# Kernel tuning notes

Hardware: AMD Instinct MI355X
Metric: run time of the kernel (lower is better)

## Reference

```python
import jax, jax.numpy as jnp
import numpy as np

EMB = 1024
FF = 4096
NE = 8
TOPK = 2
TEMP = 1.0


def setup_inputs() -> dict:
    key = jax.random.key(0)
    ks = jax.random.split(key, 8)
    s_emb = 1.0 / np.sqrt(EMB)
    s_ff = 1.0 / np.sqrt(FF)
    x = jax.random.normal(ks[0], (4, 2048, EMB), dtype=jnp.float32)
    gate_W = jax.random.uniform(ks[1], (EMB, NE), minval=-s_emb, maxval=s_emb, dtype=jnp.float32)
    gate_b = jax.random.uniform(ks[2], (NE,), minval=-s_emb, maxval=s_emb, dtype=jnp.float32)
    W1 = jax.random.uniform(ks[3], (NE, EMB, FF), minval=-s_emb, maxval=s_emb, dtype=jnp.float32)
    b1 = jax.random.uniform(ks[4], (NE, FF), minval=-s_emb, maxval=s_emb, dtype=jnp.float32)
    W2 = jax.random.uniform(ks[5], (NE, FF, EMB), minval=-s_ff, maxval=s_ff, dtype=jnp.float32)
    b2 = jax.random.uniform(ks[6], (NE, EMB), minval=-s_ff, maxval=s_ff, dtype=jnp.float32)
    return {"x": x, "gate_W": gate_W, "gate_b": gate_b, "W1": W1, "b1": b1, "W2": W2, "b2": b2}


def reference(x, gate_W, gate_b, W1, b1, W2, b2):
    B, S, D = x.shape
    xf = x.reshape(-1, D)  # [T, D]
    T = xf.shape[0]

    gate_logits = (xf @ gate_W + gate_b) / TEMP            # [T, E]
    gate_scores = jax.nn.softmax(gate_logits, axis=-1)     # [T, E]
    topk_scores, topk_idx = jax.lax.top_k(gate_scores, TOPK)
    topk_scores = topk_scores / jnp.sum(topk_scores, axis=-1, keepdims=True)

    # combine_weights[t, e] = sum_i topk_scores[t, i] * (topk_idx[t, i] == e)
    onehot = jax.nn.one_hot(topk_idx, NE, dtype=xf.dtype)  # [T, K, E]
    combine = jnp.einsum('tk,tke->te', topk_scores, onehot)  # [T, E]

    # Dense per-expert FFN (dropout is identity in eval): h = gelu(x W1 + b1); y = h W2 + b2
    h = jax.nn.gelu(jnp.einsum('td,edf->etf', xf, W1) + b1[:, None, :], approximate=False)
    y = jnp.einsum('etf,efd->etd', h, W2) + b2[:, None, :]  # [E, T, D]
    out = jnp.einsum('te,etd->td', combine, y).reshape(B, S, D)

    # Load-balance auxiliary loss
    expert_counts = jnp.sum(onehot, axis=(0, 1))            # [E]
    expert_fraction = expert_counts / (T * TOPK)
    routing_weights = jnp.mean(gate_scores, axis=0)
    aux_loss = NE * jnp.sum(expert_fraction * routing_weights)
    return out, aux_loss
```

## Files before the change

kernel.cpp:

```cpp
#include <hip/hip_runtime.h>
#include <math.h>

#define EMB 1024
#define FF  4096
#define NE  8
#define TTOK 8192

typedef __attribute__((ext_vector_type(4))) float  f32x4;
typedef __attribute__((ext_vector_type(8))) __bf16 bf16x8;

#define MAXROWS  18432

#define WS_COUNTS  0
#define WS_CURSORS 1024
#define WS_SSUM    1056
#define WS_NTILES  2080
#define WS_BASE    2084
#define WS_TILE_E  2176
#define WS_TILE_RB 2816
#define WS_TKIDX   4096
#define WS_TKW     69632
#define WS_SLOT    135168
#define WS_TOKID   200704
#define WS_ROWW    274432
#define WS_BIG2    350208

#define SZ_W1T ((size_t)NE * EMB * FF * 2)
#define SZ_W2T ((size_t)NE * EMB * FF * 2)
#define SZ_XB  ((size_t)TTOK * EMB * 2)
#define SZ_H   ((size_t)MAXROWS * FF * 2)
#define SZ_Y   ((size_t)MAXROWS * EMB * 4)

__device__ inline f32x4 fzero() { f32x4 v = {0.f, 0.f, 0.f, 0.f}; return v; }

__device__ __forceinline__ void gl16(const void* g, void* l) {
    __builtin_amdgcn_global_load_lds(
        (const __attribute__((address_space(1))) void*)g,
        (__attribute__((address_space(3))) void*)l, 16, 0, 0);
}

#define DSR(dst, addr, off) \
    asm volatile("ds_read_b128 %0, %1 offset:" #off : "=v"(dst) : "v"(addr))

__device__ __forceinline__ float gelu_f(float v) {
    float u = fabsf(v) * 0.70710678118654752f;
    float p = 1.0f + u * (0.278393f + u * (0.230389f + u * (0.000972f + u * 0.078108f)));
    p = p * p; p = p * p;
    float er = 1.0f - 1.0f / p;
    float s = (v >= 0.0f) ? er : -er;
    return 0.5f * v * (1.0f + s);
}

__global__ __launch_bounds__(256) void gate_kernel(
    const float* __restrict__ x, const float* __restrict__ gW, const float* __restrict__ gb,
    int* counts, float* ssum, int* tk_idx, float* tk_w)
{
    int wave = threadIdx.x >> 6;
    int lane = threadIdx.x & 63;
    int t = blockIdx.x * 4 + wave;

    float acc[NE];
#pragma unroll
    for (int e = 0; e < NE; e++) acc[e] = 0.f;

    const float* xr = x + (size_t)t * EMB;
#pragma unroll
    for (int i = 0; i < 4; i++) {
        int d0 = i * 256 + lane * 4;
        f32x4 xv = *(const f32x4*)(xr + d0);
#pragma unroll
        for (int j = 0; j < 4; j++) {
            const float* wrow = gW + (size_t)(d0 + j) * NE;
            float xs = xv[j];
#pragma unroll
            for (int e = 0; e < NE; e++) acc[e] += xs * wrow[e];
        }
    }
#pragma unroll
    for (int e = 0; e < NE; e++) {
#pragma unroll
        for (int off = 32; off; off >>= 1) acc[e] += __shfl_xor(acc[e], off, 64);
    }
    if (lane == 0) {
        float sc[NE];
        float m = -1e30f;
        for (int e = 0; e < NE; e++) { sc[e] = acc[e] + gb[e]; m = fmaxf(m, sc[e]); }
        float sum = 0.f;
        for (int e = 0; e < NE; e++) { sc[e] = expf(sc[e] - m); sum += sc[e]; }
        float inv = 1.f / sum;
        for (int e = 0; e < NE; e++) sc[e] *= inv;
        int i0 = 0; float s0 = sc[0];
        for (int e = 1; e < NE; e++) if (sc[e] > s0) { s0 = sc[e]; i0 = e; }
        int i1 = -1; float s1 = -1e30f;
        for (int e = 0; e < NE; e++) if (e != i0 && sc[e] > s1) { s1 = sc[e]; i1 = e; }
        float rn = 1.f / (s0 + s1);
        tk_idx[2 * t]     = i0;  tk_idx[2 * t + 1] = i1;
        tk_w[2 * t]       = s0 * rn;  tk_w[2 * t + 1] = s1 * rn;
        int slot = blockIdx.x & 31;
        atomicAdd(&counts[i0 * 32 + slot], 1);
        atomicAdd(&counts[i1 * 32 + slot], 1);
        for (int e = 0; e < NE; e++) atomicAdd(&ssum[e * 32 + slot], sc[e]);
    }
}

__global__ void route_build_kernel(const int* counts, const float* ssum,
                                   int* ntiles, int* base, int* tile_e, int* tile_rb,
                                   float* out_aux)
{
    if (threadIdx.x != 0 || blockIdx.x != 0) return;
    int total = 0, tiles = 0;
    float aux = 0.f;
    for (int e = 0; e < NE; e++) {
        int c = 0; float ss = 0.f;
        for (int j = 0; j < 32; j++) { c += counts[e * 32 + j]; ss += ssum[e * 32 + j]; }
        base[e] = total;
        int nt = (c + 255) >> 8;
        for (int i = 0; i < nt; i++) { tile_e[tiles] = e; tile_rb[tiles] = total + (i << 8); tiles++; }
        total += nt << 8;
        aux += ((float)c / (float)(TTOK * 2)) * (ss / (float)TTOK);
    }
    *ntiles = tiles;
    *out_aux = aux * (float)NE;
}

__global__ __launch_bounds__(256) void scatter_kernel(
    const int* __restrict__ tk_idx, const float* __restrict__ tk_w,
    const int* __restrict__ base, int* cursors, int* token_id, float* roww,
    int* slot_of)
{
    int t = blockIdx.x * 256 + threadIdx.x;
#pragma unroll
    for (int k = 0; k < 2; k++) {
        int e = tk_idx[2 * t + k];
        int pos = atomicAdd(&cursors[e], 1);
        int slot = base[e] + pos;
        token_id[slot] = t;
        roww[slot] = tk_w[2 * t + k];
        slot_of[2 * t + k] = slot;
    }
}

__global__ __launch_bounds__(256) void combine_kernel(
    const float* __restrict__ y0, const float* __restrict__ y1, int nsplit,
    const int* __restrict__ slot_of,
    const int* __restrict__ tk_idx, const float* __restrict__ tk_w,
    const float* __restrict__ b2, float* __restrict__ out)
{
    int t = blockIdx.x;
    int dq = threadIdx.x * 4;
    int s0 = slot_of[2 * t], s1 = slot_of[2 * t + 1];
    int e0 = tk_idx[2 * t], e1 = tk_idx[2 * t + 1];
    float w0 = tk_w[2 * t], w1 = tk_w[2 * t + 1];
    f32x4 ya = *(const f32x4*)(y0 + (size_t)s0 * EMB + dq);
    f32x4 yb = *(const f32x4*)(y0 + (size_t)s1 * EMB + dq);
    if (nsplit == 2) {
        f32x4 za = *(const f32x4*)(y1 + (size_t)s0 * EMB + dq);
        f32x4 zb = *(const f32x4*)(y1 + (size_t)s1 * EMB + dq);
#pragma unroll
        for (int q = 0; q < 4; q++) { ya[q] += za[q]; yb[q] += zb[q]; }
    }
    f32x4 ba = *(const f32x4*)(b2 + (size_t)e0 * EMB + dq);
    f32x4 bb = *(const f32x4*)(b2 + (size_t)e1 * EMB + dq);
    f32x4 r;
#pragma unroll
    for (int q = 0; q < 4; q++) r[q] = w0 * (ya[q] + ba[q]) + w1 * (yb[q] + bb[q]);
    *(f32x4*)(out + (size_t)t * EMB + dq) = r;
}

__global__ __launch_bounds__(256) void cvt_x_kernel(const float* __restrict__ x, __bf16* __restrict__ xb)
{
    size_t i = ((size_t)blockIdx.x * 256 + threadIdx.x) * 8;
    f32x4 a = *(const f32x4*)(x + i);
    f32x4 b = *(const f32x4*)(x + i + 4);
    bf16x8 o;
#pragma unroll
    for (int q = 0; q < 4; q++) { o[q] = (__bf16)a[q]; o[q + 4] = (__bf16)b[q]; }
    *(bf16x8*)(xb + i) = o;
}

__global__ __launch_bounds__(256) void transpose_cvt_kernel(
    const float* __restrict__ in, __bf16* __restrict__ outb, int R, int C)
{
    int e = blockIdx.z;
    const float* src = in + (size_t)e * R * C;
    __bf16* dst = outb + (size_t)e * R * C;
    __shared__ __bf16 Ls[64 * 72];
    int t = threadIdx.x;
    int r0 = blockIdx.x * 64, c0 = blockIdx.y * 64;
    int ri = t >> 4, cj = (t & 15) * 4;
#pragma unroll
    for (int p = 0; p < 4; p++) {
        int r = ri + p * 16;
        f32x4 v = *(const f32x4*)(src + (size_t)(r0 + r) * C + c0 + cj);
#pragma unroll
        for (int q = 0; q < 4; q++) Ls[(cj + q) * 72 + r] = (__bf16)v[q];
    }
    __syncthreads();
    int c = t >> 2, rq = (t & 3) * 16;
    bf16x8 a = *(bf16x8*)&Ls[c * 72 + rq];
    bf16x8 b = *(bf16x8*)&Ls[c * 72 + rq + 8];
    *(bf16x8*)(dst + (size_t)(c0 + c) * R + r0 + rq) = a;
    *(bf16x8*)(dst + (size_t)(c0 + c) * R + r0 + rq + 8) = b;
}


__global__ __launch_bounds__(512, 2) void gemm1_8p(
    const __bf16* __restrict__ xb, const __bf16* __restrict__ W1T,
    const float* __restrict__ b1,
    const int* __restrict__ token_id, const int* __restrict__ tile_e,
    const int* __restrict__ tile_rb, const int* __restrict__ ntiles,
    __bf16* __restrict__ h)
{
    extern __shared__ __bf16 lds[];
    int flat = blockIdx.x;
    int c8 = flat & 7, r = flat >> 3;
    int mti = r >> 4, nb = r & 15;
    int mt = c8 * 9 + mti;
    if (mt >= *ntiles) return;
    int e = tile_e[mt], rb = tile_rb[mt];
    int n0 = nb * 256;

    int tid = threadIdx.x, lane = tid & 63, wid = tid >> 6;
    int wr = wid >> 2, wc = wid & 3;
    int cl = lane & 15, cq = lane >> 4;

    int srow = tid >> 2;
    int schunk = (tid & 3) ^ ((tid >> 3) & 3);
    const __bf16* ag[2];
#pragma unroll
    for (int hm = 0; hm < 2; hm++) {
        int tok = token_id[rb + hm * 128 + srow];
        if (tok < 0) tok = 0;
        ag[hm] = xb + (size_t)tok * EMB + schunk * 8;
    }
    const __bf16* bg[2];
#pragma unroll
    for (int hn = 0; hn < 2; hn++)
        bg[hn] = W1T + ((size_t)e * FF + (size_t)(n0 + hn * 128 + srow)) * EMB + schunk * 8;

    int sdA0 = wid * 512, sdA1 = 4096 + wid * 512;
    int sdB0 = 8192 + wid * 512, sdB1 = 12288 + wid * 512;

    uint32_t lb = (uint32_t)(uintptr_t)(__attribute__((address_space(3))) __bf16*)lds;
    int xoffe = (cq ^ ((cl >> 1) & 3)) * 8;
    uint32_t ab0 = lb + 2u * (uint32_t)(wr * 4096 + cl * 32 + xoffe);
    uint32_t bb0 = lb + 2u * (uint32_t)(8192 + (wc >> 1) * 4096 + ((wc & 1) * 64 + cl) * 32 + xoffe);

    f32x4 acc[8][4];
#pragma unroll
    for (int i = 0; i < 8; i++)
#pragma unroll
        for (int j = 0; j < 4; j++) acc[i][j] = fzero();

    const int NT = EMB / 32;
#pragma unroll
    for (int t0 = 0; t0 < 3; t0++) {
        __bf16* bp = lds + t0 * 16384;
        int k0 = t0 * 32;
        gl16(ag[0] + k0, bp + sdA0);
        gl16(ag[1] + k0, bp + sdA1);
        gl16(bg[0] + k0, bp + sdB0);
        gl16(bg[1] + k0, bp + sdB1);
    }
    asm volatile("s_waitcnt vmcnt(8)" ::: "memory");
    __builtin_amdgcn_s_barrier();

#pragma unroll 1
    for (int t = 0; t < NT; t++) {
        uint32_t cboff = (uint32_t)(t & 3) * 32768u;
        uint32_t aaddr = ab0 + cboff, baddr = bb0 + cboff;
        bf16x8 b[4], a[8];
        DSR(b[0], baddr, 0);    DSR(b[1], baddr, 1024);
        DSR(b[2], baddr, 2048); DSR(b[3], baddr, 3072);
        DSR(a[0], aaddr, 0);    DSR(a[1], aaddr, 1024);
        DSR(a[2], aaddr, 2048); DSR(a[3], aaddr, 3072);
        DSR(a[4], aaddr, 4096); DSR(a[5], aaddr, 5120);
        DSR(a[6], aaddr, 6144); DSR(a[7], aaddr, 7168);

        int kt = t + 3;
        if (kt < NT) {
            __bf16* sp = lds + (kt & 3) * 16384;
            int ko = kt * 32;
            gl16(ag[0] + ko, sp + sdA0);
            gl16(ag[1] + ko, sp + sdA1);
            gl16(bg[0] + ko, sp + sdB0);
            gl16(bg[1] + ko, sp + sdB1);
        }

        asm volatile("s_waitcnt lgkmcnt(0)" ::: "memory");
        __builtin_amdgcn_sched_barrier(0);
        __builtin_amdgcn_s_setprio(1);
#pragma unroll
        for (int mi = 0; mi < 8; mi++)
#pragma unroll
            for (int ni = 0; ni < 4; ni++)
                acc[mi][ni] = __builtin_amdgcn_mfma_f32_16x16x32_bf16(a[mi], b[ni], acc[mi][ni], 0, 0, 0);
        __builtin_amdgcn_s_setprio(0);

        if (t < NT - 3)       { asm volatile("s_waitcnt vmcnt(8)" ::: "memory"); }
        else if (t == NT - 3) { asm volatile("s_waitcnt vmcnt(4)" ::: "memory"); }
        else if (t == NT - 2) { asm volatile("s_waitcnt vmcnt(0)" ::: "memory"); }
        if (t < NT - 1) __builtin_amdgcn_s_barrier();
    }

    const float* b1g = b1 + (size_t)e * FF + n0;
#pragma unroll
    for (int mi = 0; mi < 8; mi++) {
#pragma unroll
        for (int ni = 0; ni < 4; ni++) {
            int col = wc * 64 + ni * 16 + cl;
            float bias = b1g[col];
#pragma unroll
            for (int j = 0; j < 4; j++) {
                int row = wr * 128 + mi * 16 + cq * 4 + j;
                float v = acc[mi][ni][j] + bias;
                h[(size_t)(rb + row) * FF + n0 + col] = (__bf16)gelu_f(v);
            }
        }
    }
}

__global__ __launch_bounds__(512, 2) void gemm2_8p(
    const __bf16* __restrict__ h, const __bf16* __restrict__ W2T,
    const int* __restrict__ tile_e, const int* __restrict__ tile_rb,
    const int* __restrict__ ntiles,
    float* __restrict__ y0, float* __restrict__ y1, int nsplit)
{
    extern __shared__ __bf16 lds[];
    int flat = blockIdx.x;
    int c8 = flat & 7, r = flat >> 3;
    int z = r / 36; int r36 = r - z * 36;
    int mti = r36 >> 2, nb = r36 & 3;
    int mt = c8 * 9 + mti;
    if (mt >= *ntiles) return;
    int e = tile_e[mt], rb = tile_rb[mt];
    int n0 = nb * 256;
    int KC = FF / nsplit;
    int koff = z * KC;
    float* y = z ? y1 : y0;

    int tid = threadIdx.x, lane = tid & 63, wid = tid >> 6;
    int wr = wid >> 2, wc = wid & 3;
    int cl = lane & 15, cq = lane >> 4;

    int srow = tid >> 2;
    int schunk = (tid & 3) ^ ((tid >> 3) & 3);
    const __bf16* ag[2];
#pragma unroll
    for (int hm = 0; hm < 2; hm++)
        ag[hm] = h + (size_t)(rb + hm * 128 + srow) * FF + koff + schunk * 8;
    const __bf16* bg[2];
#pragma unroll
    for (int hn = 0; hn < 2; hn++)
        bg[hn] = W2T + ((size_t)e * EMB + (size_t)(n0 + hn * 128 + srow)) * FF + koff + schunk * 8;

    int sdA0 = wid * 512, sdA1 = 4096 + wid * 512;
    int sdB0 = 8192 + wid * 512, sdB1 = 12288 + wid * 512;

    uint32_t lb = (uint32_t)(uintptr_t)(__attribute__((address_space(3))) __bf16*)lds;
    int xoffe = (cq ^ ((cl >> 1) & 3)) * 8;
    uint32_t ab0 = lb + 2u * (uint32_t)(wr * 4096 + cl * 32 + xoffe);
    uint32_t bb0 = lb + 2u * (uint32_t)(8192 + (wc >> 1) * 4096 + ((wc & 1) * 64 + cl) * 32 + xoffe);

    f32x4 acc[8][4];
#pragma unroll
    for (int i = 0; i < 8; i++)
#pragma unroll
        for (int j = 0; j < 4; j++) acc[i][j] = fzero();

    const int NT = KC / 32;
#pragma unroll
    for (int t0 = 0; t0 < 3; t0++) {
        __bf16* bp = lds + t0 * 16384;
        int k0 = t0 * 32;
        gl16(ag[0] + k0, bp + sdA0);
        gl16(ag[1] + k0, bp + sdA1);
        gl16(bg[0] + k0, bp + sdB0);
        gl16(bg[1] + k0, bp + sdB1);
    }
    asm volatile("s_waitcnt vmcnt(8)" ::: "memory");
    __builtin_amdgcn_s_barrier();

#pragma unroll 1
    for (int t = 0; t < NT; t++) {
        uint32_t cboff = (uint32_t)(t & 3) * 32768u;
        uint32_t aaddr = ab0 + cboff, baddr = bb0 + cboff;
        bf16x8 b[4], a[8];
        DSR(b[0], baddr, 0);    DSR(b[1], baddr, 1024);
        DSR(b[2], baddr, 2048); DSR(b[3], baddr, 3072);
        DSR(a[0], aaddr, 0);    DSR(a[1], aaddr, 1024);
        DSR(a[2], aaddr, 2048); DSR(a[3], aaddr, 3072);
        DSR(a[4], aaddr, 4096); DSR(a[5], aaddr, 5120);
        DSR(a[6], aaddr, 6144); DSR(a[7], aaddr, 7168);

        int kt = t + 3;
        if (kt < NT) {
            __bf16* sp = lds + (kt & 3) * 16384;
            int ko = kt * 32;
            gl16(ag[0] + ko, sp + sdA0);
            gl16(ag[1] + ko, sp + sdA1);
            gl16(bg[0] + ko, sp + sdB0);
            gl16(bg[1] + ko, sp + sdB1);
        }

        asm volatile("s_waitcnt lgkmcnt(0)" ::: "memory");
        __builtin_amdgcn_sched_barrier(0);
        __builtin_amdgcn_s_setprio(1);
#pragma unroll
        for (int mi = 0; mi < 8; mi++)
#pragma unroll
            for (int ni = 0; ni < 4; ni++)
                acc[mi][ni] = __builtin_amdgcn_mfma_f32_16x16x32_bf16(a[mi], b[ni], acc[mi][ni], 0, 0, 0);
        __builtin_amdgcn_s_setprio(0);

        if (t < NT - 3)       { asm volatile("s_waitcnt vmcnt(8)" ::: "memory"); }
        else if (t == NT - 3) { asm volatile("s_waitcnt vmcnt(4)" ::: "memory"); }
        else if (t == NT - 2) { asm volatile("s_waitcnt vmcnt(0)" ::: "memory"); }
        if (t < NT - 1) __builtin_amdgcn_s_barrier();
    }

#pragma unroll
    for (int mi = 0; mi < 8; mi++) {
#pragma unroll
        for (int ni = 0; ni < 4; ni++) {
            int col = wc * 64 + ni * 16 + cl;
#pragma unroll
            for (int j = 0; j < 4; j++) {
                int row = wr * 128 + mi * 16 + cq * 4 + j;
                y[(size_t)(rb + row) * EMB + n0 + col] = acc[mi][ni][j];
            }
        }
    }
}

extern "C" void kernel_launch(void* const* d_in, const int* in_sizes, int n_in,
                              void* d_out, int out_size, void* d_ws, size_t ws_size,
                              hipStream_t stream)
{
    const float* x   = (const float*)d_in[0];
    const float* gW  = (const float*)d_in[1];
    const float* gb  = (const float*)d_in[2];
    const float* W1  = (const float*)d_in[3];
    const float* b1  = (const float*)d_in[4];
    const float* W2  = (const float*)d_in[5];
    const float* b2  = (const float*)d_in[6];
    float* out = (float*)d_out;

    char* ws = (char*)d_ws;
    int*   counts  = (int*)(ws + WS_COUNTS);
    int*   cursors = (int*)(ws + WS_CURSORS);
    float* ssum    = (float*)(ws + WS_SSUM);
    int*   ntiles  = (int*)(ws + WS_NTILES);
    int*   base    = (int*)(ws + WS_BASE);
    int*   tile_e  = (int*)(ws + WS_TILE_E);
    int*   tile_rb = (int*)(ws + WS_TILE_RB);
    int*   tk_idx  = (int*)(ws + WS_TKIDX);
    float* tk_w    = (float*)(ws + WS_TKW);
    int*   slot_of = (int*)(ws + WS_SLOT);
    int*   token_id= (int*)(ws + WS_TOKID);
    float* roww    = (float*)(ws + WS_ROWW);

    __bf16* W1T  = (__bf16*)(ws + WS_BIG2);
    __bf16* xb   = (__bf16*)(ws + WS_BIG2 + SZ_W1T);
    __bf16* W2T  = (__bf16*)(ws + WS_BIG2 + SZ_W1T + SZ_XB);
    __bf16* hbuf = (__bf16*)(ws + WS_BIG2 + SZ_W1T + SZ_XB + SZ_W2T);
    size_t fixedend = WS_BIG2 + SZ_W1T + SZ_XB + SZ_W2T;

    float* y0 = (float*)(ws + WS_BIG2);
    float* y1 = (float*)(ws + fixedend + SZ_H);
    int nsplit = (ws_size >= fixedend + SZ_H + SZ_Y) ? 2 : 1;

    hipFuncSetAttribute((const void*)gemm1_8p, hipFuncAttributeMaxDynamicSharedMemorySize, 131072);
    hipFuncSetAttribute((const void*)gemm2_8p, hipFuncAttributeMaxDynamicSharedMemorySize, 131072);

    hipMemsetAsync(ws + WS_COUNTS, 0, 2080, stream);
    hipMemsetAsync(ws + WS_TOKID, 0xFF, (size_t)MAXROWS * 4, stream);

    cvt_x_kernel<<<TTOK * EMB / 2048, 256, 0, stream>>>(x, xb);
    transpose_cvt_kernel<<<dim3(EMB / 64, FF / 64, NE), 256, 0, stream>>>(W1, W1T, EMB, FF);
    transpose_cvt_kernel<<<dim3(FF / 64, EMB / 64, NE), 256, 0, stream>>>(W2, W2T, FF, EMB);

    gate_kernel<<<TTOK / 4, 256, 0, stream>>>(x, gW, gb, counts, ssum, tk_idx, tk_w);
    route_build_kernel<<<1, 64, 0, stream>>>(counts, ssum, ntiles, base, tile_e, tile_rb,
                                             out + (size_t)TTOK * EMB);
    scatter_kernel<<<TTOK / 256, 256, 0, stream>>>(tk_idx, tk_w, base, cursors, token_id, roww, slot_of);

    gemm1_8p<<<8 * 9 * 16, 512, 131072, stream>>>(
        xb, W1T, b1, token_id, tile_e, tile_rb, ntiles, hbuf);
    gemm2_8p<<<8 * 9 * 4 * nsplit, 512, 131072, stream>>>(
        hbuf, W2T, tile_e, tile_rb, ntiles, y0, y1, nsplit);
    combine_kernel<<<TTOK, 256, 0, stream>>>(y0, y1, nsplit, slot_of, tk_idx, tk_w, b2, out);
}
```

Baseline: 712.4 us.

## Switch GEMM mainloops to double-buffered 64-wide K steps with split LDS waits

Both expert GEMM kernels now consume 64 K-elements per iteration from two LDS buffers, replacing the previous four-stage ring of 32-wide tiles. The next iteration's global loads are issued at the top of each iteration. The first 32-wide half's MFMAs start after a partial lgkmcnt wait, so they can overlap the remaining LDS reads. This halves the number of barriers and loop iterations, but the prefetch distance drops from three tiles to one and the loop waits for vmcnt(0) each iteration, which may expose global-load latency. Keeping both halves' fragments live also raises register pressure.

```diff
diff --git a/kernel.cpp b/kernel.cpp
--- a/kernel.cpp
+++ b/kernel.cpp
@@ -252,40 +252,60 @@
 #pragma unroll
         for (int j = 0; j < 4; j++) acc[i][j] = fzero();
 
-    const int NT = EMB / 32;
-#pragma unroll
-    for (int t0 = 0; t0 < 3; t0++) {
-        __bf16* bp = lds + t0 * 16384;
-        int k0 = t0 * 32;
+    const int NT = EMB / 64;
+#pragma unroll
+    for (int s = 0; s < 2; s++) {
+        __bf16* bp = lds + s * 16384;
+        int k0 = s * 32;
         gl16(ag[0] + k0, bp + sdA0);
         gl16(ag[1] + k0, bp + sdA1);
         gl16(bg[0] + k0, bp + sdB0);
         gl16(bg[1] + k0, bp + sdB1);
     }
-    asm volatile("s_waitcnt vmcnt(8)" ::: "memory");
+    asm volatile("s_waitcnt vmcnt(0)" ::: "memory");
     __builtin_amdgcn_s_barrier();
 
 #pragma unroll 1
     for (int t = 0; t < NT; t++) {
-        uint32_t cboff = (uint32_t)(t & 3) * 32768u;
+        int kt = t + 1;
+        if (kt < NT) {
+            __bf16* bufp = lds + (kt & 1) * 32768;
+#pragma unroll
+            for (int s = 0; s < 2; s++) {
+                __bf16* bp = bufp + s * 16384;
+                int ko = kt * 64 + s * 32;
+                gl16(ag[0] + ko, bp + sdA0);
+                gl16(ag[1] + ko, bp + sdA1);
+                gl16(bg[0] + ko, bp + sdB0);
+                gl16(bg[1] + ko, bp + sdB1);
+            }
+        }
+
+        uint32_t cboff = (uint32_t)(t & 1) * 65536u;
         uint32_t aaddr = ab0 + cboff, baddr = bb0 + cboff;
-        bf16x8 b[4], a[8];
-        DSR(b[0], baddr, 0);    DSR(b[1], baddr, 1024);
-        DSR(b[2], baddr, 2048); DSR(b[3], baddr, 3072);
-        DSR(a[0], aaddr, 0);    DSR(a[1], aaddr, 1024);
-        DSR(a[2], aaddr, 2048); DSR(a[3], aaddr, 3072);
-        DSR(a[4], aaddr, 4096); DSR(a[5], aaddr, 5120);
-        DSR(a[6], aaddr, 6144); DSR(a[7], aaddr, 7168);
-
-        int kt = t + 3;
-        if (kt < NT) {
-            __bf16* sp = lds + (kt & 3) * 16384;
-            int ko = kt * 32;
-            gl16(ag[0] + ko, sp + sdA0);
-            gl16(ag[1] + ko, sp + sdA1);
-            gl16(bg[0] + ko, sp + sdB0);
-            gl16(bg[1] + ko, sp + sdB1);
-        }
+        bf16x8 b0[4], a0[8], b1v[4], a1[8];
+        DSR(b0[0], baddr, 0);     DSR(b0[1], baddr, 1024);
+        DSR(b0[2], baddr, 2048);  DSR(b0[3], baddr, 3072);
+        DSR(a0[0], aaddr, 0);     DSR(a0[1], aaddr, 1024);
+        DSR(a0[2], aaddr, 2048);  DSR(a0[3], aaddr, 3072);
+        DSR(a0[4], aaddr, 4096);  DSR(a0[5], aaddr, 5120);
+        DSR(a0[6], aaddr, 6144);  DSR(a0[7], aaddr, 7168);
+        DSR(b1v[0], baddr, 32768); DSR(b1v[1], baddr, 33792);
+        DSR(b1v[2], baddr, 34816); DSR(b1v[3], baddr, 35840);
+        DSR(a1[0], aaddr, 32768); DSR(a1[1], aaddr, 33792);
+        DSR(a1[2], aaddr, 34816); DSR(a1[3], aaddr, 35840);
+        DSR(a1[4], aaddr, 36864); DSR(a1[5], aaddr, 37888);
+        DSR(a1[6], aaddr, 38912); DSR(a1[7], aaddr, 39936);
+
+        asm volatile("s_waitcnt lgkmcnt(12)" ::: "memory");
+        __builtin_amdgcn_sched_barrier(0);
+        __builtin_amdgcn_s_setprio(1);
+#pragma unroll
+        for (int mi = 0; mi < 8; mi++)
+#pragma unroll
+            for (int ni = 0; ni < 4; ni++)
+                acc[mi][ni] = __builtin_amdgcn_mfma_f32_16x16x32_bf16(a0[mi], b0[ni], acc[mi][ni], 0, 0, 0);
+        __builtin_amdgcn_s_setprio(0);
 
         asm volatile("s_waitcnt lgkmcnt(0)" ::: "memory");
         __builtin_amdgcn_sched_barrier(0);
@@ -294,12 +314,10 @@
         for (int mi = 0; mi < 8; mi++)
 #pragma unroll
             for (int ni = 0; ni < 4; ni++)
-                acc[mi][ni] = __builtin_amdgcn_mfma_f32_16x16x32_bf16(a[mi], b[ni], acc[mi][ni], 0, 0, 0);
+                acc[mi][ni] = __builtin_amdgcn_mfma_f32_16x16x32_bf16(a1[mi], b1v[ni], acc[mi][ni], 0, 0, 0);
         __builtin_amdgcn_s_setprio(0);
 
-        if (t < NT - 3)       { asm volatile("s_waitcnt vmcnt(8)" ::: "memory"); }
-        else if (t == NT - 3) { asm volatile("s_waitcnt vmcnt(4)" ::: "memory"); }
-        else if (t == NT - 2) { asm volatile("s_waitcnt vmcnt(0)" ::: "memory"); }
+        asm volatile("s_waitcnt vmcnt(0)" ::: "memory");
         if (t < NT - 1) __builtin_amdgcn_s_barrier();
     }
 
@@ -368,40 +386,60 @@
 #pragma unroll
         for (int j = 0; j < 4; j++) acc[i][j] = fzero();
 
-    const int NT = KC / 32;
-#pragma unroll
-    for (int t0 = 0; t0 < 3; t0++) {
-        __bf16* bp = lds + t0 * 16384;
-        int k0 = t0 * 32;
+    const int NT = KC / 64;
+#pragma unroll
+    for (int s = 0; s < 2; s++) {
+        __bf16* bp = lds + s * 16384;
+        int k0 = s * 32;
         gl16(ag[0] + k0, bp + sdA0);
         gl16(ag[1] + k0, bp + sdA1);
         gl16(bg[0] + k0, bp + sdB0);
         gl16(bg[1] + k0, bp + sdB1);
     }
-    asm volatile("s_waitcnt vmcnt(8)" ::: "memory");
+    asm volatile("s_waitcnt vmcnt(0)" ::: "memory");
     __builtin_amdgcn_s_barrier();
 
 #pragma unroll 1
     for (int t = 0; t < NT; t++) {
-        uint32_t cboff = (uint32_t)(t & 3) * 32768u;
+        int kt = t + 1;
+        if (kt < NT) {
+            __bf16* bufp = lds + (kt & 1) * 32768;
+#pragma unroll
+            for (int s = 0; s < 2; s++) {
+                __bf16* bp = bufp + s * 16384;
+                int ko = kt * 64 + s * 32;
+                gl16(ag[0] + ko, bp + sdA0);
+                gl16(ag[1] + ko, bp + sdA1);
+                gl16(bg[0] + ko, bp + sdB0);
+                gl16(bg[1] + ko, bp + sdB1);
+            }
+        }
+
+        uint32_t cboff = (uint32_t)(t & 1) * 65536u;
         uint32_t aaddr = ab0 + cboff, baddr = bb0 + cboff;
-        bf16x8 b[4], a[8];
-        DSR(b[0], baddr, 0);    DSR(b[1], baddr, 1024);
-        DSR(b[2], baddr, 2048); DSR(b[3], baddr, 3072);
-        DSR(a[0], aaddr, 0);    DSR(a[1], aaddr, 1024);
-        DSR(a[2], aaddr, 2048); DSR(a[3], aaddr, 3072);
-        DSR(a[4], aaddr, 4096); DSR(a[5], aaddr, 5120);
-        DSR(a[6], aaddr, 6144); DSR(a[7], aaddr, 7168);
-
-        int kt = t + 3;
-        if (kt < NT) {
-            __bf16* sp = lds + (kt & 3) * 16384;
-            int ko = kt * 32;
-            gl16(ag[0] + ko, sp + sdA0);
-            gl16(ag[1] + ko, sp + sdA1);
-            gl16(bg[0] + ko, sp + sdB0);
-            gl16(bg[1] + ko, sp + sdB1);
-        }
+        bf16x8 b0[4], a0[8], b1v[4], a1[8];
+        DSR(b0[0], baddr, 0);     DSR(b0[1], baddr, 1024);
+        DSR(b0[2], baddr, 2048);  DSR(b0[3], baddr, 3072);
+        DSR(a0[0], aaddr, 0);     DSR(a0[1], aaddr, 1024);
+        DSR(a0[2], aaddr, 2048);  DSR(a0[3], aaddr, 3072);
+        DSR(a0[4], aaddr, 4096);  DSR(a0[5], aaddr, 5120);
+        DSR(a0[6], aaddr, 6144);  DSR(a0[7], aaddr, 7168);
+        DSR(b1v[0], baddr, 32768); DSR(b1v[1], baddr, 33792);
+        DSR(b1v[2], baddr, 34816); DSR(b1v[3], baddr, 35840);
+        DSR(a1[0], aaddr, 32768); DSR(a1[1], aaddr, 33792);
+        DSR(a1[2], aaddr, 34816); DSR(a1[3], aaddr, 35840);
+        DSR(a1[4], aaddr, 36864); DSR(a1[5], aaddr, 37888);
+        DSR(a1[6], aaddr, 38912); DSR(a1[7], aaddr, 39936);
+
+        asm volatile("s_waitcnt lgkmcnt(12)" ::: "memory");
+        __builtin_amdgcn_sched_barrier(0);
+        __builtin_amdgcn_s_setprio(1);
+#pragma unroll
+        for (int mi = 0; mi < 8; mi++)
+#pragma unroll
+            for (int ni = 0; ni < 4; ni++)
+                acc[mi][ni] = __builtin_amdgcn_mfma_f32_16x16x32_bf16(a0[mi], b0[ni], acc[mi][ni], 0, 0, 0);
+        __builtin_amdgcn_s_setprio(0);
 
         asm volatile("s_waitcnt lgkmcnt(0)" ::: "memory");
         __builtin_amdgcn_sched_barrier(0);
@@ -410,12 +448,10 @@
         for (int mi = 0; mi < 8; mi++)
 #pragma unroll
             for (int ni = 0; ni < 4; ni++)
-                acc[mi][ni] = __builtin_amdgcn_mfma_f32_16x16x32_bf16(a[mi], b[ni], acc[mi][ni], 0, 0, 0);
+                acc[mi][ni] = __builtin_amdgcn_mfma_f32_16x16x32_bf16(a1[mi], b1v[ni], acc[mi][ni], 0, 0, 0);
         __builtin_amdgcn_s_setprio(0);
 
-        if (t < NT - 3)       { asm volatile("s_waitcnt vmcnt(8)" ::: "memory"); }
-        else if (t == NT - 3) { asm volatile("s_waitcnt vmcnt(4)" ::: "memory"); }
-        else if (t == NT - 2) { asm volatile("s_waitcnt vmcnt(0)" ::: "memory"); }
+        asm volatile("s_waitcnt vmcnt(0)" ::: "memory");
         if (t < NT - 1) __builtin_amdgcn_s_barrier();
     }
 
```

After: 721.2 us. About the same (+1.2%).

## Replace split-K gemm2 with 128x128 single-buffered tile kernel; stagger gemm1 LDS waits

Applied to the files above, without the earlier changes.

The second expert GEMM drops its 256x256 four-stage pipelined kernel with optional split-K and uses a simpler 128x128-tile kernel with 256 threads, single LDS buffer and syncthreads per K step. It launches many more blocks and needs no second partial buffer, so the combine kernel reads only one y buffer. Separately, gemm1's MFMA block is split into four groups, each waiting on a progressively smaller lgkmcnt so compute overlaps the remaining LDS reads. The new gemm2 gives up software pipelining and the larger tile's data reuse, which may expose global load latency.

```diff
diff --git a/kernel.cpp b/kernel.cpp
--- a/kernel.cpp
+++ b/kernel.cpp
@@ -28,8 +28,6 @@
 #define SZ_W1T ((size_t)NE * EMB * FF * 2)
 #define SZ_W2T ((size_t)NE * EMB * FF * 2)
 #define SZ_XB  ((size_t)TTOK * EMB * 2)
-#define SZ_H   ((size_t)MAXROWS * FF * 2)
-#define SZ_Y   ((size_t)MAXROWS * EMB * 4)
 
 __device__ inline f32x4 fzero() { f32x4 v = {0.f, 0.f, 0.f, 0.f}; return v; }
 
@@ -141,7 +139,7 @@
 }
 
 __global__ __launch_bounds__(256) void combine_kernel(
-    const float* __restrict__ y0, const float* __restrict__ y1, int nsplit,
+    const float* __restrict__ y0,
     const int* __restrict__ slot_of,
     const int* __restrict__ tk_idx, const float* __restrict__ tk_w,
     const float* __restrict__ b2, float* __restrict__ out)
@@ -153,12 +151,6 @@
     float w0 = tk_w[2 * t], w1 = tk_w[2 * t + 1];
     f32x4 ya = *(const f32x4*)(y0 + (size_t)s0 * EMB + dq);
     f32x4 yb = *(const f32x4*)(y0 + (size_t)s1 * EMB + dq);
-    if (nsplit == 2) {
-        f32x4 za = *(const f32x4*)(y1 + (size_t)s0 * EMB + dq);
-        f32x4 zb = *(const f32x4*)(y1 + (size_t)s1 * EMB + dq);
-#pragma unroll
-        for (int q = 0; q < 4; q++) { ya[q] += za[q]; yb[q] += zb[q]; }
-    }
     f32x4 ba = *(const f32x4*)(b2 + (size_t)e0 * EMB + dq);
     f32x4 bb = *(const f32x4*)(b2 + (size_t)e1 * EMB + dq);
     f32x4 r;
@@ -202,7 +194,6 @@
     *(bf16x8*)(dst + (size_t)(c0 + c) * R + r0 + rq) = a;
     *(bf16x8*)(dst + (size_t)(c0 + c) * R + r0 + rq + 8) = b;
 }
-
 
 __global__ __launch_bounds__(512, 2) void gemm1_8p(
     const __bf16* __restrict__ xb, const __bf16* __restrict__ W1T,
@@ -287,11 +278,32 @@
             gl16(bg[1] + ko, sp + sdB1);
         }
 
+        asm volatile("s_waitcnt lgkmcnt(6)" ::: "memory");
+        __builtin_amdgcn_sched_barrier(0);
+        __builtin_amdgcn_s_setprio(1);
+#pragma unroll
+        for (int mi = 0; mi < 2; mi++)
+#pragma unroll
+            for (int ni = 0; ni < 4; ni++)
+                acc[mi][ni] = __builtin_amdgcn_mfma_f32_16x16x32_bf16(a[mi], b[ni], acc[mi][ni], 0, 0, 0);
+        asm volatile("s_waitcnt lgkmcnt(4)" ::: "memory");
+        __builtin_amdgcn_sched_barrier(0);
+#pragma unroll
+        for (int mi = 2; mi < 4; mi++)
+#pragma unroll
+            for (int ni = 0; ni < 4; ni++)
+                acc[mi][ni] = __builtin_amdgcn_mfma_f32_16x16x32_bf16(a[mi], b[ni], acc[mi][ni], 0, 0, 0);
+        asm volatile("s_waitcnt lgkmcnt(2)" ::: "memory");
+        __builtin_amdgcn_sched_barrier(0);
+#pragma unroll
+        for (int mi = 4; mi < 6; mi++)
+#pragma unroll
+            for (int ni = 0; ni < 4; ni++)
+                acc[mi][ni] = __builtin_amdgcn_mfma_f32_16x16x32_bf16(a[mi], b[ni], acc[mi][ni], 0, 0, 0);
         asm volatile("s_waitcnt lgkmcnt(0)" ::: "memory");
         __builtin_amdgcn_sched_barrier(0);
-        __builtin_amdgcn_s_setprio(1);
-#pragma unroll
-        for (int mi = 0; mi < 8; mi++)
+#pragma unroll
+        for (int mi = 6; mi < 8; mi++)
 #pragma unroll
             for (int ni = 0; ni < 4; ni++)
                 acc[mi][ni] = __builtin_amdgcn_mfma_f32_16x16x32_bf16(a[mi], b[ni], acc[mi][ni], 0, 0, 0);
@@ -320,113 +332,75 @@
     }
 }
 
-__global__ __launch_bounds__(512, 2) void gemm2_8p(
+__global__ __launch_bounds__(256) void gemm2_m97(
     const __bf16* __restrict__ h, const __bf16* __restrict__ W2T,
     const int* __restrict__ tile_e, const int* __restrict__ tile_rb,
-    const int* __restrict__ ntiles,
-    float* __restrict__ y0, float* __restrict__ y1, int nsplit)
-{
-    extern __shared__ __bf16 lds[];
+    const int* __restrict__ ntiles, float* __restrict__ y)
+{
+    __shared__ __bf16 As[128 * 32];
+    __shared__ __bf16 Bs[128 * 32];
+
     int flat = blockIdx.x;
     int c8 = flat & 7, r = flat >> 3;
-    int z = r / 36; int r36 = r - z * 36;
-    int mti = r36 >> 2, nb = r36 & 3;
-    int mt = c8 * 9 + mti;
-    if (mt >= *ntiles) return;
-    int e = tile_e[mt], rb = tile_rb[mt];
-    int n0 = nb * 256;
-    int KC = FF / nsplit;
-    int koff = z * KC;
-    float* y = z ? y1 : y0;
+    int sti = r >> 3, nb = r & 7;
+    int st = c8 * 18 + sti;
+    int nt2 = *ntiles * 2;
+    if (st >= nt2) return;
+    int e = tile_e[st >> 1];
+    int rb = tile_rb[st >> 1] + (st & 1) * 128;
+    int n0 = nb * 128;
 
     int tid = threadIdx.x, lane = tid & 63, wid = tid >> 6;
-    int wr = wid >> 2, wc = wid & 3;
+    int wr = wid >> 1, wc = wid & 1;
     int cl = lane & 15, cq = lane >> 4;
 
-    int srow = tid >> 2;
-    int schunk = (tid & 3) ^ ((tid >> 3) & 3);
-    const __bf16* ag[2];
-#pragma unroll
-    for (int hm = 0; hm < 2; hm++)
-        ag[hm] = h + (size_t)(rb + hm * 128 + srow) * FF + koff + schunk * 8;
-    const __bf16* bg[2];
-#pragma unroll
-    for (int hn = 0; hn < 2; hn++)
-        bg[hn] = W2T + ((size_t)e * EMB + (size_t)(n0 + hn * 128 + srow)) * FF + koff + schunk * 8;
-
-    int sdA0 = wid * 512, sdA1 = 4096 + wid * 512;
-    int sdB0 = 8192 + wid * 512, sdB1 = 12288 + wid * 512;
-
-    uint32_t lb = (uint32_t)(uintptr_t)(__attribute__((address_space(3))) __bf16*)lds;
-    int xoffe = (cq ^ ((cl >> 1) & 3)) * 8;
-    uint32_t ab0 = lb + 2u * (uint32_t)(wr * 4096 + cl * 32 + xoffe);
-    uint32_t bb0 = lb + 2u * (uint32_t)(8192 + (wc >> 1) * 4096 + ((wc & 1) * 64 + cl) * 32 + xoffe);
-
-    f32x4 acc[8][4];
-#pragma unroll
-    for (int i = 0; i < 8; i++)
+    int arow = (wid << 5) + (lane >> 2);
+    int chk = (lane & 3) * 8;
+    const __bf16* a0s = h + (size_t)(rb + arow) * FF + chk;
+    const __bf16* a1s = h + (size_t)(rb + arow + 16) * FF + chk;
+    const __bf16* b0s = W2T + ((size_t)e * EMB + (size_t)(n0 + arow)) * FF + chk;
+    const __bf16* b1s = W2T + ((size_t)e * EMB + (size_t)(n0 + arow + 16)) * FF + chk;
+    __bf16* dA0 = As + wid * 1024;
+    __bf16* dA1 = As + wid * 1024 + 512;
+    __bf16* dB0 = Bs + wid * 1024;
+    __bf16* dB1 = Bs + wid * 1024 + 512;
+
+    f32x4 acc[4][4];
+#pragma unroll
+    for (int i = 0; i < 4; i++)
 #pragma unroll
         for (int j = 0; j < 4; j++) acc[i][j] = fzero();
 
-    const int NT = KC / 32;
-#pragma unroll
-    for (int t0 = 0; t0 < 3; t0++) {
-        __bf16* bp = lds + t0 * 16384;
-        int k0 = t0 * 32;
-        gl16(ag[0] + k0, bp + sdA0);
-        gl16(ag[1] + k0, bp + sdA1);
-        gl16(bg[0] + k0, bp + sdB0);
-        gl16(bg[1] + k0, bp + sdB1);
-    }
-    asm volatile("s_waitcnt vmcnt(8)" ::: "memory");
-    __builtin_amdgcn_s_barrier();
-
-#pragma unroll 1
-    for (int t = 0; t < NT; t++) {
-        uint32_t cboff = (uint32_t)(t & 3) * 32768u;
-        uint32_t aaddr = ab0 + cboff, baddr = bb0 + cboff;
-        bf16x8 b[4], a[8];
-        DSR(b[0], baddr, 0);    DSR(b[1], baddr, 1024);
-        DSR(b[2], baddr, 2048); DSR(b[3], baddr, 3072);
-        DSR(a[0], aaddr, 0);    DSR(a[1], aaddr, 1024);
-        DSR(a[2], aaddr, 2048); DSR(a[3], aaddr, 3072);
-        DSR(a[4], aaddr, 4096); DSR(a[5], aaddr, 5120);
-        DSR(a[6], aaddr, 6144); DSR(a[7], aaddr, 7168);
-
-        int kt = t + 3;
-        if (kt < NT) {
-            __bf16* sp = lds + (kt & 3) * 16384;
-            int ko = kt * 32;
-            gl16(ag[0] + ko, sp + sdA0);
-            gl16(ag[1] + ko, sp + sdA1);
-            gl16(bg[0] + ko, sp + sdB0);
-            gl16(bg[1] + ko, sp + sdB1);
-        }
-
-        asm volatile("s_waitcnt lgkmcnt(0)" ::: "memory");
-        __builtin_amdgcn_sched_barrier(0);
-        __builtin_amdgcn_s_setprio(1);
-#pragma unroll
-        for (int mi = 0; mi < 8; mi++)
+    for (int k0 = 0; k0 < FF; k0 += 32) {
+        gl16(a0s + k0, dA0);
+        gl16(a1s + k0, dA1);
+        gl16(b0s + k0, dB0);
+        gl16(b1s + k0, dB1);
+        __syncthreads();
+
+        bf16x8 af[4], bv[4];
+#pragma unroll
+        for (int mi = 0; mi < 4; mi++)
+            af[mi] = *(const bf16x8*)&As[(wr * 64 + mi * 16 + cl) * 32 + cq * 8];
+#pragma unroll
+        for (int ni = 0; ni < 4; ni++)
+            bv[ni] = *(const bf16x8*)&Bs[(wc * 64 + ni * 16 + cl) * 32 + cq * 8];
+#pragma unroll
+        for (int mi = 0; mi < 4; mi++)
 #pragma unroll
             for (int ni = 0; ni < 4; ni++)
-                acc[mi][ni] = __builtin_amdgcn_mfma_f32_16x16x32_bf16(a[mi], b[ni], acc[mi][ni], 0, 0, 0);
-        __builtin_amdgcn_s_setprio(0);
-
-        if (t < NT - 3)       { asm volatile("s_waitcnt vmcnt(8)" ::: "memory"); }
-        else if (t == NT - 3) { asm volatile("s_waitcnt vmcnt(4)" ::: "memory"); }
-        else if (t == NT - 2) { asm volatile("s_waitcnt vmcnt(0)" ::: "memory"); }
-        if (t < NT - 1) __builtin_amdgcn_s_barrier();
-    }
-
-#pragma unroll
-    for (int mi = 0; mi < 8; mi++) {
+                acc[mi][ni] = __builtin_amdgcn_mfma_f32_16x16x32_bf16(af[mi], bv[ni], acc[mi][ni], 0, 0, 0);
+        __syncthreads();
+    }
+
+#pragma unroll
+    for (int mi = 0; mi < 4; mi++) {
 #pragma unroll
         for (int ni = 0; ni < 4; ni++) {
             int col = wc * 64 + ni * 16 + cl;
 #pragma unroll
             for (int j = 0; j < 4; j++) {
-                int row = wr * 128 + mi * 16 + cq * 4 + j;
+                int row = wr * 64 + mi * 16 + cq * 4 + j;
                 y[(size_t)(rb + row) * EMB + n0 + col] = acc[mi][ni][j];
             }
         }
@@ -464,14 +438,10 @@
     __bf16* xb   = (__bf16*)(ws + WS_BIG2 + SZ_W1T);
     __bf16* W2T  = (__bf16*)(ws + WS_BIG2 + SZ_W1T + SZ_XB);
     __bf16* hbuf = (__bf16*)(ws + WS_BIG2 + SZ_W1T + SZ_XB + SZ_W2T);
-    size_t fixedend = WS_BIG2 + SZ_W1T + SZ_XB + SZ_W2T;
 
     float* y0 = (float*)(ws + WS_BIG2);
-    float* y1 = (float*)(ws + fixedend + SZ_H);
-    int nsplit = (ws_size >= fixedend + SZ_H + SZ_Y) ? 2 : 1;
 
     hipFuncSetAttribute((const void*)gemm1_8p, hipFuncAttributeMaxDynamicSharedMemorySize, 131072);
-    hipFuncSetAttribute((const void*)gemm2_8p, hipFuncAttributeMaxDynamicSharedMemorySize, 131072);
 
     hipMemsetAsync(ws + WS_COUNTS, 0, 2080, stream);
     hipMemsetAsync(ws + WS_TOKID, 0xFF, (size_t)MAXROWS * 4, stream);
@@ -487,7 +457,7 @@
 
     gemm1_8p<<<8 * 9 * 16, 512, 131072, stream>>>(
         xb, W1T, b1, token_id, tile_e, tile_rb, ntiles, hbuf);
-    gemm2_8p<<<8 * 9 * 4 * nsplit, 512, 131072, stream>>>(
-        hbuf, W2T, tile_e, tile_rb, ntiles, y0, y1, nsplit);
-    combine_kernel<<<TTOK, 256, 0, stream>>>(y0, y1, nsplit, slot_of, tk_idx, tk_w, b2, out);
-}
+    gemm2_m97<<<8 * 18 * 8, 256, 0, stream>>>(
+        hbuf, W2T, tile_e, tile_rb, ntiles, y0);
+    combine_kernel<<<TTOK, 256, 0, stream>>>(y0, slot_of, tk_idx, tk_w, b2, out);
+}
```

After: 810.9 us. 13.8% more time.

## Split GEMM K-step into four barriered MFMA phases and fuse x conversion into gate

Applied to the files above, without the earlier changes.

Both expert GEMM main loops now split each K-step into four MFMA phases. LDS reads and the global-to-LDS prefetches are interleaved between the phases, each phase bracketed by workgroup barriers and priority changes, in the style of a ping-pong schedule. The aim is to overlap LDS and global traffic with matrix-core work and lower register pressure, since only half the A fragments are live at once. It adds several barriers per iteration, which may cost more than the overlap gains. Separately, the fp32-to-bf16 conversion of x is folded into the gate kernel, which already reads x, removing one kernel launch and one full read of x.

```diff
diff --git a/kernel.cpp b/kernel.cpp
--- a/kernel.cpp
+++ b/kernel.cpp
@@ -8,6 +8,7 @@
 
 typedef __attribute__((ext_vector_type(4))) float  f32x4;
 typedef __attribute__((ext_vector_type(8))) __bf16 bf16x8;
+typedef __attribute__((ext_vector_type(4))) __bf16 bf16x4;
 
 #define MAXROWS  18432
 
@@ -42,6 +43,16 @@
 #define DSR(dst, addr, off) \
     asm volatile("ds_read_b128 %0, %1 offset:" #off : "=v"(dst) : "v"(addr))
 
+#define PHASE_HEAD() \
+    __builtin_amdgcn_s_barrier(); \
+    asm volatile("s_waitcnt lgkmcnt(0)" ::: "memory"); \
+    __builtin_amdgcn_sched_barrier(0); \
+    __builtin_amdgcn_s_setprio(1);
+
+#define PHASE_TAIL() \
+    __builtin_amdgcn_s_setprio(0); \
+    __builtin_amdgcn_s_barrier();
+
 __device__ __forceinline__ float gelu_f(float v) {
     float u = fabsf(v) * 0.70710678118654752f;
     float p = 1.0f + u * (0.278393f + u * (0.230389f + u * (0.000972f + u * 0.078108f)));
@@ -53,7 +64,7 @@
 
 __global__ __launch_bounds__(256) void gate_kernel(
     const float* __restrict__ x, const float* __restrict__ gW, const float* __restrict__ gb,
-    int* counts, float* ssum, int* tk_idx, float* tk_w)
+    int* counts, float* ssum, int* tk_idx, float* tk_w, __bf16* __restrict__ xb)
 {
     int wave = threadIdx.x >> 6;
     int lane = threadIdx.x & 63;
@@ -64,10 +75,15 @@
     for (int e = 0; e < NE; e++) acc[e] = 0.f;
 
     const float* xr = x + (size_t)t * EMB;
+    __bf16* xbr = xb + (size_t)t * EMB;
 #pragma unroll
     for (int i = 0; i < 4; i++) {
         int d0 = i * 256 + lane * 4;
         f32x4 xv = *(const f32x4*)(xr + d0);
+        bf16x4 cv;
+#pragma unroll
+        for (int q = 0; q < 4; q++) cv[q] = (__bf16)xv[q];
+        *(bf16x4*)(xbr + d0) = cv;
 #pragma unroll
         for (int j = 0; j < 4; j++) {
             const float* wrow = gW + (size_t)(d0 + j) * NE;
@@ -167,17 +183,6 @@
     *(f32x4*)(out + (size_t)t * EMB + dq) = r;
 }
 
-__global__ __launch_bounds__(256) void cvt_x_kernel(const float* __restrict__ x, __bf16* __restrict__ xb)
-{
-    size_t i = ((size_t)blockIdx.x * 256 + threadIdx.x) * 8;
-    f32x4 a = *(const f32x4*)(x + i);
-    f32x4 b = *(const f32x4*)(x + i + 4);
-    bf16x8 o;
-#pragma unroll
-    for (int q = 0; q < 4; q++) { o[q] = (__bf16)a[q]; o[q + 4] = (__bf16)b[q]; }
-    *(bf16x8*)(xb + i) = o;
-}
-
 __global__ __launch_bounds__(256) void transpose_cvt_kernel(
     const float* __restrict__ in, __bf16* __restrict__ outb, int R, int C)
 {
@@ -269,38 +274,54 @@
     for (int t = 0; t < NT; t++) {
         uint32_t cboff = (uint32_t)(t & 3) * 32768u;
         uint32_t aaddr = ab0 + cboff, baddr = bb0 + cboff;
-        bf16x8 b[4], a[8];
+        int kt = t + 3;
+        bool st = (kt < NT);
+        __bf16* sp = lds + (kt & 3) * 16384;
+        int ko = kt * 32;
+
+        bf16x8 b[4], a[4], a2[4];
         DSR(b[0], baddr, 0);    DSR(b[1], baddr, 1024);
-        DSR(b[2], baddr, 2048); DSR(b[3], baddr, 3072);
         DSR(a[0], aaddr, 0);    DSR(a[1], aaddr, 1024);
         DSR(a[2], aaddr, 2048); DSR(a[3], aaddr, 3072);
-        DSR(a[4], aaddr, 4096); DSR(a[5], aaddr, 5120);
-        DSR(a[6], aaddr, 6144); DSR(a[7], aaddr, 7168);
-
-        int kt = t + 3;
-        if (kt < NT) {
-            __bf16* sp = lds + (kt & 3) * 16384;
-            int ko = kt * 32;
-            gl16(ag[0] + ko, sp + sdA0);
-            gl16(ag[1] + ko, sp + sdA1);
-            gl16(bg[0] + ko, sp + sdB0);
-            gl16(bg[1] + ko, sp + sdB1);
-        }
-
-        asm volatile("s_waitcnt lgkmcnt(0)" ::: "memory");
-        __builtin_amdgcn_sched_barrier(0);
-        __builtin_amdgcn_s_setprio(1);
-#pragma unroll
-        for (int mi = 0; mi < 8; mi++)
-#pragma unroll
-            for (int ni = 0; ni < 4; ni++)
+        if (st) gl16(ag[0] + ko, sp + sdA0);
+        PHASE_HEAD()
+#pragma unroll
+        for (int mi = 0; mi < 4; mi++)
+#pragma unroll
+            for (int ni = 0; ni < 2; ni++)
                 acc[mi][ni] = __builtin_amdgcn_mfma_f32_16x16x32_bf16(a[mi], b[ni], acc[mi][ni], 0, 0, 0);
-        __builtin_amdgcn_s_setprio(0);
-
+        PHASE_TAIL()
+        DSR(b[2], baddr, 2048); DSR(b[3], baddr, 3072);
+        if (st) gl16(ag[1] + ko, sp + sdA1);
+        PHASE_HEAD()
+#pragma unroll
+        for (int mi = 0; mi < 4; mi++)
+#pragma unroll
+            for (int ni = 2; ni < 4; ni++)
+                acc[mi][ni] = __builtin_amdgcn_mfma_f32_16x16x32_bf16(a[mi], b[ni], acc[mi][ni], 0, 0, 0);
+        PHASE_TAIL()
+        DSR(a2[0], aaddr, 4096); DSR(a2[1], aaddr, 5120);
+        DSR(a2[2], aaddr, 6144); DSR(a2[3], aaddr, 7168);
+        if (st) gl16(bg[0] + ko, sp + sdB0);
+        PHASE_HEAD()
+#pragma unroll
+        for (int mi = 0; mi < 4; mi++)
+#pragma unroll
+            for (int ni = 2; ni < 4; ni++)
+                acc[4 + mi][ni] = __builtin_amdgcn_mfma_f32_16x16x32_bf16(a2[mi], b[ni], acc[4 + mi][ni], 0, 0, 0);
+        PHASE_TAIL()
+        if (st) gl16(bg[1] + ko, sp + sdB1);
         if (t < NT - 3)       { asm volatile("s_waitcnt vmcnt(8)" ::: "memory"); }
         else if (t == NT - 3) { asm volatile("s_waitcnt vmcnt(4)" ::: "memory"); }
         else if (t == NT - 2) { asm volatile("s_waitcnt vmcnt(0)" ::: "memory"); }
-        if (t < NT - 1) __builtin_amdgcn_s_barrier();
+        __builtin_amdgcn_s_barrier();
+        __builtin_amdgcn_s_setprio(1);
+#pragma unroll
+        for (int mi = 0; mi < 4; mi++)
+#pragma unroll
+            for (int ni = 0; ni < 2; ni++)
+                acc[4 + mi][ni] = __builtin_amdgcn_mfma_f32_16x16x32_bf16(a2[mi], b[ni], acc[4 + mi][ni], 0, 0, 0);
+        PHASE_TAIL()
     }
 
     const float* b1g = b1 + (size_t)e * FF + n0;
@@ -385,38 +406,54 @@
     for (int t = 0; t < NT; t++) {
         uint32_t cboff = (uint32_t)(t & 3) * 32768u;
         uint32_t aaddr = ab0 + cboff, baddr = bb0 + cboff;
-        bf16x8 b[4], a[8];
+        int kt = t + 3;
+        bool st = (kt < NT);
+        __bf16* sp = lds + (kt & 3) * 16384;
+        int ko = kt * 32;
+
+        bf16x8 b[4], a[4], a2[4];
         DSR(b[0], baddr, 0);    DSR(b[1], baddr, 1024);
-        DSR(b[2], baddr, 2048); DSR(b[3], baddr, 3072);
         DSR(a[0], aaddr, 0);    DSR(a[1], aaddr, 1024);
         DSR(a[2], aaddr, 2048); DSR(a[3], aaddr, 3072);
-        DSR(a[4], aaddr, 4096); DSR(a[5], aaddr, 5120);
-        DSR(a[6], aaddr, 6144); DSR(a[7], aaddr, 7168);
-
-        int kt = t + 3;
-        if (kt < NT) {
-            __bf16* sp = lds + (kt & 3) * 16384;
-            int ko = kt * 32;
-            gl16(ag[0] + ko, sp + sdA0);
-            gl16(ag[1] + ko, sp + sdA1);
-            gl16(bg[0] + ko, sp + sdB0);
-            gl16(bg[1] + ko, sp + sdB1);
-        }
-
-        asm volatile("s_waitcnt lgkmcnt(0)" ::: "memory");
-        __builtin_amdgcn_sched_barrier(0);
-        __builtin_amdgcn_s_setprio(1);
-#pragma unroll
-        for (int mi = 0; mi < 8; mi++)
-#pragma unroll
-            for (int ni = 0; ni < 4; ni++)
+        if (st) gl16(ag[0] + ko, sp + sdA0);
+        PHASE_HEAD()
+#pragma unroll
+        for (int mi = 0; mi < 4; mi++)
+#pragma unroll
+            for (int ni = 0; ni < 2; ni++)
                 acc[mi][ni] = __builtin_amdgcn_mfma_f32_16x16x32_bf16(a[mi], b[ni], acc[mi][ni], 0, 0, 0);
-        __builtin_amdgcn_s_setprio(0);
-
+        PHASE_TAIL()
+        DSR(b[2], baddr, 2048); DSR(b[3], baddr, 3072);
+        if (st) gl16(ag[1] + ko, sp + sdA1);
+        PHASE_HEAD()
+#pragma unroll
+        for (int mi = 0; mi < 4; mi++)
+#pragma unroll
+            for (int ni = 2; ni < 4; ni++)
+                acc[mi][ni] = __builtin_amdgcn_mfma_f32_16x16x32_bf16(a[mi], b[ni], acc[mi][ni], 0, 0, 0);
+        PHASE_TAIL()
+        DSR(a2[0], aaddr, 4096); DSR(a2[1], aaddr, 5120);
+        DSR(a2[2], aaddr, 6144); DSR(a2[3], aaddr, 7168);
+        if (st) gl16(bg[0] + ko, sp + sdB0);
+        PHASE_HEAD()
+#pragma unroll
+        for (int mi = 0; mi < 4; mi++)
+#pragma unroll
+            for (int ni = 2; ni < 4; ni++)
+                acc[4 + mi][ni] = __builtin_amdgcn_mfma_f32_16x16x32_bf16(a2[mi], b[ni], acc[4 + mi][ni], 0, 0, 0);
+        PHASE_TAIL()
+        if (st) gl16(bg[1] + ko, sp + sdB1);
         if (t < NT - 3)       { asm volatile("s_waitcnt vmcnt(8)" ::: "memory"); }
         else if (t == NT - 3) { asm volatile("s_waitcnt vmcnt(4)" ::: "memory"); }
         else if (t == NT - 2) { asm volatile("s_waitcnt vmcnt(0)" ::: "memory"); }
-        if (t < NT - 1) __builtin_amdgcn_s_barrier();
+        __builtin_amdgcn_s_barrier();
+        __builtin_amdgcn_s_setprio(1);
+#pragma unroll
+        for (int mi = 0; mi < 4; mi++)
+#pragma unroll
+            for (int ni = 0; ni < 2; ni++)
+                acc[4 + mi][ni] = __builtin_amdgcn_mfma_f32_16x16x32_bf16(a2[mi], b[ni], acc[4 + mi][ni], 0, 0, 0);
+        PHASE_TAIL()
     }
 
 #pragma unroll
@@ -476,11 +513,10 @@
     hipMemsetAsync(ws + WS_COUNTS, 0, 2080, stream);
     hipMemsetAsync(ws + WS_TOKID, 0xFF, (size_t)MAXROWS * 4, stream);
 
-    cvt_x_kernel<<<TTOK * EMB / 2048, 256, 0, stream>>>(x, xb);
     transpose_cvt_kernel<<<dim3(EMB / 64, FF / 64, NE), 256, 0, stream>>>(W1, W1T, EMB, FF);
     transpose_cvt_kernel<<<dim3(FF / 64, EMB / 64, NE), 256, 0, stream>>>(W2, W2T, FF, EMB);
 
-    gate_kernel<<<TTOK / 4, 256, 0, stream>>>(x, gW, gb, counts, ssum, tk_idx, tk_w);
+    gate_kernel<<<TTOK / 4, 256, 0, stream>>>(x, gW, gb, counts, ssum, tk_idx, tk_w, xb);
     route_build_kernel<<<1, 64, 0, stream>>>(counts, ssum, ntiles, base, tile_e, tile_rb,
                                              out + (size_t)TTOK * EMB);
     scatter_kernel<<<TTOK / 256, 256, 0, stream>>>(tk_idx, tk_w, base, cursors, token_id, roww, slot_of);
```

Result: no change. 705.8 us (-0.9%).
